# Kernel tuning notes

Measured on AMD Instinct MI355X. Metric: run time of the kernel, lower is better.

Reference implementation:

```python
import jax, jax.numpy as jnp
import numpy as np

N, C, L, K = 150000, 256, 50000, 200  # nodes, classes(=feature dim), labeled count, top-k


def setup_inputs() -> dict:
    key = jax.random.key(0)
    k1, k2 = jax.random.split(key)
    inputs = jax.random.normal(k1, (N, C), dtype=jnp.float32)
    cls = jax.random.randint(k2, (N,), 0, C)
    labels = jax.nn.one_hot(cls, C, dtype=jnp.float32)  # one-hot label matrix [N, C]
    labels_mask = jnp.arange(N) < L      # first L nodes labeled
    unlabels_mask = ~labels_mask
    return {"inputs": inputs, "labels": labels, "labels_mask": labels_mask,
            "unlabels_mask": unlabels_mask, "k": K}


def _l2n(x):
    # tf.nn.l2_normalize with epsilon 1e-12
    return x * jax.lax.rsqrt(jnp.maximum(jnp.sum(x * x, axis=-1, keepdims=True), 1e-12))


def reference(inputs, labels, labels_mask, unlabels_mask, k):
    lm = labels_mask.astype(inputs.dtype)    # [N]
    um = unlabels_mask.astype(inputs.dtype)  # [N]
    # protos: per-class mean of labeled features (masked matmul == boolean_mask + matmul)
    total = jnp.einsum('nf,nc->fc', inputs * lm[:, None], labels)  # [F, C]
    weight = 1.0 / jnp.sum(labels, 0)                               # 1/count per class (over ALL labels, as in TF)
    protos = (total * weight[None, :]).T                            # [C, F]
    # cosine similarity of every node to every prototype [N, C]
    prob = _l2n(inputs) @ _l2n(protos).T
    # per-row top-k, scattered back to a sparse [N, C] (raw top values, softmax in TF was dead code)
    vals, idx = jax.lax.top_k(prob, k)                              # [N, k]
    rows = jnp.arange(prob.shape[0])[:, None]
    sparse = jnp.zeros_like(prob).at[rows, idx].set(vals)
    p = sparse * um[:, None]                                        # only unlabeled rows contribute
    # per-class normalization: denom_c = sum_u p[u,c] + n_labeled_c
    denom = jnp.sum(p, 0) + jnp.sum(labels * lm[:, None], 0)        # [C]
    w = p / denom[None, :]                                          # [N, C]
    # change[c] = sum_u w[u,c] * (x_u - protos[c])
    change = w.T @ inputs - jnp.sum(w, 0)[:, None] * protos         # [C, F]
    protos = protos + change
    logits = _l2n(inputs) @ _l2n(protos).T                          # [N, C]
    return logits
```

## Files before the change

kernel.cpp:

```cpp
#include <hip/hip_runtime.h>

typedef unsigned int uint;
typedef unsigned short ushort;
typedef float f32x4 __attribute__((ext_vector_type(4)));
typedef uint u32x4 __attribute__((ext_vector_type(4)));
typedef uint u32x2 __attribute__((ext_vector_type(2)));
typedef __bf16 bf16x8 __attribute__((ext_vector_type(8)));

constexpr int NR = 150000;
constexpr int CD = 256;
constexpr int LR = 50000;
constexpr int KEX = 56;
constexpr int NB1 = 49984;
constexpr int NUP = 100032;
constexpr int NTP = 150080;

__device__ __forceinline__ ushort f2bf(float x) {
  uint u = __builtin_bit_cast(uint, x);
  u += 0x7FFFu + ((u >> 16) & 1u);
  return (ushort)(u >> 16);
}
__device__ __forceinline__ uint key16(uint b) {
  return (b & 0x8000u) ? (~b & 0xFFFFu) : (b | 0x8000u);
}

__global__ __launch_bounds__(256) void k_cls(const float* __restrict__ labels,
                                             int* __restrict__ cls,
                                             float* __restrict__ ca,
                                             float* __restrict__ cl) {
  __shared__ int ha[256], hl[256];
  int t = threadIdx.x;
  ha[t] = 0; hl[t] = 0;
  __syncthreads();
  int lane = t & 63;
  int wid = (blockIdx.x << 2) | (t >> 6);
  int nw = gridDim.x << 2;
  for (int n = wid; n < NR; n += nw) {
    f32x4 v = *reinterpret_cast<const f32x4*>(&labels[n * CD + lane * 4]);
    int j = v[0] > 0.5f ? 0 : v[1] > 0.5f ? 1 : v[2] > 0.5f ? 2 : v[3] > 0.5f ? 3 : -1;
    if (j >= 0) {
      int c = lane * 4 + j;
      cls[n] = c;
      atomicAdd(&ha[c], 1);
      if (n < LR) atomicAdd(&hl[c], 1);
    }
  }
  __syncthreads();
  atomicAdd(&ca[t], (float)ha[t]);
  atomicAdd(&cl[t], (float)hl[t]);
}

__global__ __launch_bounds__(256) void k_prep(const float* __restrict__ X,
                                              ushort* __restrict__ Xt,
                                              float* __restrict__ invn) {
  __shared__ __align__(16) ushort xl[64 * 264];
  __shared__ float red[256];
  int t = threadIdx.x;
  int r = t >> 2, cq = t & 3;
  int g0 = blockIdx.x * 64;
  int g = g0 + r;
  bool valid = g < NR;
  float ss = 0.f;
#pragma unroll
  for (int j = 0; j < 16; ++j) {
    int col = cq * 4 + j * 16;
    f32x4 x = valid ? *reinterpret_cast<const f32x4*>(&X[g * CD + col])
                    : (f32x4){0.f, 0.f, 0.f, 0.f};
    ss += x[0] * x[0] + x[1] * x[1] + x[2] * x[2] + x[3] * x[3];
    uint p0 = (uint)f2bf(x[0]) | ((uint)f2bf(x[1]) << 16);
    uint p1 = (uint)f2bf(x[2]) | ((uint)f2bf(x[3]) << 16);
    *reinterpret_cast<u32x2*>(&xl[r * 264 + col]) = (u32x2){p0, p1};
  }
  red[t] = ss;
  __syncthreads();
  if (t < 64) {
    float s4 = red[t * 4] + red[t * 4 + 1] + red[t * 4 + 2] + red[t * 4 + 3];
    if (g0 + t < NR) invn[g0 + t] = rsqrtf(fmaxf(s4, 1e-12f));
  }
  ushort* xp = Xt + (size_t)blockIdx.x * 16384;
  int f = t;
  uint buf[4];
  for (int n = 0; n < 64; ++n) {
    ushort v16 = xl[n * 264 + f];
    int sl = n & 7;
    if (sl & 1) buf[sl >> 1] |= (uint)v16 << 16; else buf[sl >> 1] = v16;
    if (sl == 7)
      *reinterpret_cast<u32x4*>(&xp[f * 64 + n - 7]) =
          (u32x4){buf[0], buf[1], buf[2], buf[3]};
  }
}

template <int KIND>
__global__ __launch_bounds__(1024) void k_gemmB(const int* __restrict__ cls,
                                                const ushort* __restrict__ Ap,
                                                const ushort* __restrict__ Xt,
                                                float* __restrict__ P,
                                                int nch, int nbase) {
  __shared__ __align__(16) ushort Al[256 * 40];
  __shared__ __align__(16) ushort Bl[256 * 40];
  int t = threadIdx.x;
  int lane = t & 63, w = t >> 6;
  int m = lane & 15, qd = lane >> 4;
  f32x4 acc[16];
#pragma unroll
  for (int i = 0; i < 16; ++i) acc[i] = (f32x4){0.f, 0.f, 0.f, 0.f};

  for (int ch = blockIdx.x; ch < nch; ch += gridDim.x) {
    int n0 = ch * 32;
    __syncthreads();
    if (KIND == 0) {
      for (int i = t; i < 5120; i += 1024) reinterpret_cast<uint*>(Al)[i] = 0u;
      __syncthreads();
      if (t < 32) {
        int g = n0 + t;
        if (g < LR) Al[cls[g] * 40 + t] = 0x3F80;
      }
    } else {
      const ushort* ap = Ap + (size_t)(n0 >> 6) * 16384 + (n0 & 63);
      int c = t >> 2, off = (t & 3) * 8;
      *reinterpret_cast<u32x4*>(&Al[c * 40 + off]) =
          *reinterpret_cast<const u32x4*>(&ap[c * 64 + off]);
    }
    {
      int gr = nbase + n0;
      const ushort* xp = Xt + (size_t)(gr >> 6) * 16384 + (gr & 63);
      int fR = t >> 2, off = (t & 3) * 8;
      *reinterpret_cast<u32x4*>(&Bl[fR * 40 + off]) =
          *reinterpret_cast<const u32x4*>(&xp[fR * 64 + off]);
    }
    __syncthreads();
    bf16x8 a = *reinterpret_cast<const bf16x8*>(&Al[(w * 16 + m) * 40 + qd * 8]);
#pragma unroll
    for (int ft = 0; ft < 16; ++ft) {
      bf16x8 b = *reinterpret_cast<const bf16x8*>(&Bl[(ft * 16 + m) * 40 + qd * 8]);
      acc[ft] = __builtin_amdgcn_mfma_f32_16x16x32_bf16(a, b, acc[ft], 0, 0, 0);
    }
  }
  float* Ps = P + (size_t)blockIdx.x * 65536;
#pragma unroll
  for (int ft = 0; ft < 16; ++ft)
#pragma unroll
    for (int r = 0; r < 4; ++r)
      Ps[(w * 16 + qd * 4 + r) * 256 + ft * 16 + m] = acc[ft][r];
}

__global__ __launch_bounds__(256) void k_protos(const float* __restrict__ P, int nsl,
                                                const float* __restrict__ ca,
                                                float* __restrict__ protos,
                                                ushort* __restrict__ phat) {
  __shared__ float red[256];
  int c = blockIdx.x, f = threadIdx.x;
  float s = 0.f;
  for (int i = 0; i < nsl; ++i) s += P[i * 65536 + c * 256 + f];
  float cnt = ca[c];
  float pv = cnt > 0.5f ? s / cnt : 0.f;
  protos[c * 256 + f] = pv;
  red[f] = pv * pv;
  __syncthreads();
  for (int st = 128; st > 0; st >>= 1) {
    if (f < st) red[f] += red[f + st];
    __syncthreads();
  }
  float iv = rsqrtf(fmaxf(red[0], 1e-12f));
  phat[c * 256 + f] = f2bf(pv * iv);
}

__global__ __launch_bounds__(256) void k_update(const float* __restrict__ PS, int nsl,
                                                const float* __restrict__ protos,
                                                const float* __restrict__ q,
                                                const float* __restrict__ clab,
                                                ushort* __restrict__ phat2) {
  __shared__ float red[256];
  int c = blockIdx.x, f = threadIdx.x;
  float s = 0.f;
  for (int i = 0; i < nsl; ++i) s += PS[i * 65536 + c * 256 + f];
  float qc = q[c];
  float den = qc + clab[c];
  float pv = protos[c * 256 + f];
  float np = pv + (s - qc * pv) / den;
  red[f] = np * np;
  __syncthreads();
  for (int st = 128; st > 0; st >>= 1) {
    if (f < st) red[f] += red[f + st];
    __syncthreads();
  }
  float iv = rsqrtf(fmaxf(red[0], 1e-12f));
  phat2[c * 256 + f] = f2bf(np * iv);
}

template <int TOPK>
__global__ __launch_bounds__(256) void k_passA(const float* __restrict__ X,
                                               const float* __restrict__ invn,
                                               const ushort* __restrict__ Bm,
                                               float* __restrict__ out,
                                               ushort* __restrict__ pt,
                                               float* __restrict__ q,
                                               int gbase) {
  __shared__ __align__(16) ushort Al[64 * 40];
  __shared__ __align__(16) ushort Bl[256 * 40];
  __shared__ __align__(16) ushort s16[TOPK ? 64 * 272 : 64];
  __shared__ uint tkey[TOPK ? 64 : 1];
  int t = threadIdx.x;
  int lane = t & 63, w = t >> 6;
  int m = lane & 15, qd = lane >> 4;
  int g0 = gbase + blockIdx.x * 64;
  int row = t >> 2, off = (t & 3) * 8;
  int g = g0 + row;
  bool valid = g < NR;
  float inv = valid ? invn[g] : 0.f;
  f32x4 acc[16];
#pragma unroll
  for (int i = 0; i < 16; ++i) acc[i] = (f32x4){0.f, 0.f, 0.f, 0.f};

  for (int k0 = 0; k0 < 256; k0 += 32) {
    __syncthreads();
    f32x4 x0 = valid ? *reinterpret_cast<const f32x4*>(&X[g * CD + k0 + off])
                     : (f32x4){0.f, 0.f, 0.f, 0.f};
    f32x4 x1 = valid ? *reinterpret_cast<const f32x4*>(&X[g * CD + k0 + off + 4])
                     : (f32x4){0.f, 0.f, 0.f, 0.f};
    x0 *= inv; x1 *= inv;
    uint u0 = (uint)f2bf(x0[0]) | ((uint)f2bf(x0[1]) << 16);
    uint u1 = (uint)f2bf(x0[2]) | ((uint)f2bf(x0[3]) << 16);
    uint u2 = (uint)f2bf(x1[0]) | ((uint)f2bf(x1[1]) << 16);
    uint u3 = (uint)f2bf(x1[2]) | ((uint)f2bf(x1[3]) << 16);
    *reinterpret_cast<u32x4*>(&Al[row * 40 + off]) = (u32x4){u0, u1, u2, u3};
#pragma unroll
    for (int i = 0; i < 4; ++i) {
      int c = (t >> 2) + i * 64;
      *reinterpret_cast<u32x4*>(&Bl[c * 40 + off]) =
          *reinterpret_cast<const u32x4*>(&Bm[c * 256 + k0 + off]);
    }
    __syncthreads();
    bf16x8 a = *reinterpret_cast<const bf16x8*>(&Al[(w * 16 + m) * 40 + qd * 8]);
#pragma unroll
    for (int ft = 0; ft < 16; ++ft) {
      bf16x8 b = *reinterpret_cast<const bf16x8*>(&Bl[(ft * 16 + m) * 40 + qd * 8]);
      acc[ft] = __builtin_amdgcn_mfma_f32_16x16x32_bf16(a, b, acc[ft], 0, 0, 0);
    }
  }

  if (TOPK == 0) {
#pragma unroll
    for (int ft = 0; ft < 16; ++ft)
#pragma unroll
      for (int r = 0; r < 4; ++r) {
        int rr = w * 16 + qd * 4 + r;
        int gg = g0 + rr;
        if (gg < NR) out[gg * 256 + ft * 16 + m] = acc[ft][r];
      }
  } else {
    __syncthreads();
#pragma unroll
    for (int ft = 0; ft < 16; ++ft)
#pragma unroll
      for (int r = 0; r < 4; ++r)
        s16[(w * 16 + qd * 4 + r) * 272 + ft * 16 + m] = f2bf(acc[ft][r]);
    __syncthreads();
    for (int i = 0; i < 16; ++i) {
      int rw = w * 16 + i;
      u32x2 pk = *reinterpret_cast<const u32x2*>(&s16[rw * 272 + lane * 4]);
      uint k0 = key16(pk[0] & 0xFFFFu);
      uint k1 = key16(pk[0] >> 16);
      uint k2 = key16(pk[1] & 0xFFFFu);
      uint k3 = key16(pk[1] >> 16);
      uint mth = 0u;
      for (int b = 15; b >= 0; --b) {
        uint cand = mth | (1u << b);
        int cnt = __builtin_popcountll(__ballot(k0 < cand)) +
                  __builtin_popcountll(__ballot(k1 < cand)) +
                  __builtin_popcountll(__ballot(k2 < cand)) +
                  __builtin_popcountll(__ballot(k3 < cand));
        if (cnt <= KEX) mth = cand;
      }
      if (lane == 0) tkey[rw] = mth;
    }
    __syncthreads();
    int c = t;
    float qloc = 0.f;
    uint buf[4];
    ushort* pp = pt + (size_t)blockIdx.x * 16384;
    for (int n = 0; n < 64; ++n) {
      int grow = g0 + n;
      ushort v16 = s16[n * 272 + c];
      bool keep = (key16(v16) >= tkey[n]) && (grow >= LR) && (grow < NR);
      ushort pv16 = keep ? v16 : (ushort)0;
      if (keep) qloc += __builtin_bit_cast(float, (uint)v16 << 16);
      int sl = n & 7;
      if (sl & 1) buf[sl >> 1] |= (uint)pv16 << 16; else buf[sl >> 1] = pv16;
      if (sl == 7)
        *reinterpret_cast<u32x4*>(&pp[c * 64 + n - 7]) =
            (u32x4){buf[0], buf[1], buf[2], buf[3]};
    }
    atomicAdd(&q[c], qloc);
  }
}

extern "C" void kernel_launch(void* const* d_in, const int* in_sizes, int n_in,
                              void* d_out, int out_size, void* d_ws, size_t ws_size,
                              hipStream_t stream) {
  const float* inputs = (const float*)d_in[0];
  const float* labels = (const float*)d_in[1];
  float* out = (float*)d_out;

  ushort* p_t = (ushort*)d_out;
  ushort* Xt  = (ushort*)((char*)d_out + (size_t)256 * NUP * 2);

  char* ws = (char*)d_ws;
  float* q      = (float*)(ws + 0);
  float* c_all  = (float*)(ws + 1024);
  float* c_lab  = (float*)(ws + 2048);
  float* protos = (float*)(ws + 4096);
  ushort* phat  = (ushort*)(ws + 4096 + 262144);
  ushort* phat2 = (ushort*)(ws + 4096 + 262144 + 131072);
  float* invn   = (float*)(ws + 528384);
  int*   cls    = (int*)(ws + 1128384);
  size_t base = 1736704;
  int sT = 128, sS = 256;
  while (base + (size_t)(sT + sS) * 262144ULL > ws_size) {
    if (sS > sT) sS >>= 1; else if (sT > 8) sT >>= 1; else break;
  }
  float* PT = (float*)(ws + base);
  float* PS = PT + (size_t)sT * 65536;

  hipMemsetAsync(ws, 0, 3072, stream);

  k_cls<<<1024, 256, 0, stream>>>(labels, cls, c_all, c_lab);
  k_prep<<<NTP / 64, 256, 0, stream>>>(inputs, Xt, invn);
  k_gemmB<0><<<sT, 1024, 0, stream>>>(cls, nullptr, Xt, PT, 1563, 0);
  k_protos<<<256, 256, 0, stream>>>(PT, sT, c_all, protos, phat);
  k_passA<1><<<NUP / 64, 256, 0, stream>>>(inputs, invn, phat, nullptr, p_t, q, NB1);
  k_gemmB<1><<<sS, 1024, 0, stream>>>(nullptr, p_t, Xt, PS, NUP / 32, NB1);
  k_update<<<256, 256, 0, stream>>>(PS, sS, protos, q, c_lab, phat2);
  k_passA<0><<<(NR + 63) / 64, 256, 0, stream>>>(inputs, invn, phat2, out, nullptr, nullptr, 0);
}
```

Before: 796.8 us.

## Prefetch next tiles into registers and batch top-k threshold search across rows

The GEMM kernels now load the next chunk's A/B tiles from global memory into registers while the current tile is computed, so global latency overlaps the MFMA work. In k_gemmB's one-hot path, the full LDS clear each iteration is replaced by clearing only the previously set entries. k_passA aliases its LDS buffers into one array to cut LDS footprint and adds a launch-bounds occupancy hint. Its per-row radix threshold search now handles four rows at once to expose more independent ballots. The cost is higher register pressure, which could lower occupancy or cause spills.

```diff
diff --git a/kernel.cpp b/kernel.cpp
--- a/kernel.cpp
+++ b/kernel.cpp
@@ -101,32 +101,57 @@
   int t = threadIdx.x;
   int lane = t & 63, w = t >> 6;
   int m = lane & 15, qd = lane >> 4;
+  int cR = t >> 2, off = (t & 3) * 8;
   f32x4 acc[16];
 #pragma unroll
   for (int i = 0; i < 16; ++i) acc[i] = (f32x4){0.f, 0.f, 0.f, 0.f};
 
-  for (int ch = blockIdx.x; ch < nch; ch += gridDim.x) {
+  if (KIND == 0) {
+    for (int i = t; i < 5120; i += 1024) reinterpret_cast<uint*>(Al)[i] = 0u;
+  }
+
+  u32x4 aR, bR;
+  int curc = -1, prevc = -1;
+  int ch = blockIdx.x;
+  if (ch < nch) {
     int n0 = ch * 32;
+    if (KIND == 1) {
+      const ushort* ap = Ap + (size_t)(n0 >> 6) * 16384 + (n0 & 63);
+      aR = *reinterpret_cast<const u32x4*>(&ap[cR * 64 + off]);
+    } else if (t < 32) {
+      int gg = n0 + t;
+      curc = (gg < LR) ? cls[gg] : -1;
+    }
+    int gr = nbase + n0;
+    const ushort* xp = Xt + (size_t)(gr >> 6) * 16384 + (gr & 63);
+    bR = *reinterpret_cast<const u32x4*>(&xp[cR * 64 + off]);
+  }
+
+  for (; ch < nch; ch += gridDim.x) {
     __syncthreads();
     if (KIND == 0) {
-      for (int i = t; i < 5120; i += 1024) reinterpret_cast<uint*>(Al)[i] = 0u;
-      __syncthreads();
       if (t < 32) {
-        int g = n0 + t;
-        if (g < LR) Al[cls[g] * 40 + t] = 0x3F80;
+        if (prevc >= 0) Al[prevc * 40 + t] = 0;
+        if (curc >= 0) Al[curc * 40 + t] = 0x3F80;
+        prevc = curc;
       }
     } else {
-      const ushort* ap = Ap + (size_t)(n0 >> 6) * 16384 + (n0 & 63);
-      int c = t >> 2, off = (t & 3) * 8;
-      *reinterpret_cast<u32x4*>(&Al[c * 40 + off]) =
-          *reinterpret_cast<const u32x4*>(&ap[c * 64 + off]);
-    }
-    {
+      *reinterpret_cast<u32x4*>(&Al[cR * 40 + off]) = aR;
+    }
+    *reinterpret_cast<u32x4*>(&Bl[cR * 40 + off]) = bR;
+    int chn = ch + gridDim.x;
+    if (chn < nch) {
+      int n0 = chn * 32;
+      if (KIND == 1) {
+        const ushort* ap = Ap + (size_t)(n0 >> 6) * 16384 + (n0 & 63);
+        aR = *reinterpret_cast<const u32x4*>(&ap[cR * 64 + off]);
+      } else if (t < 32) {
+        int gg = n0 + t;
+        curc = (gg < LR) ? cls[gg] : -1;
+      }
       int gr = nbase + n0;
       const ushort* xp = Xt + (size_t)(gr >> 6) * 16384 + (gr & 63);
-      int fR = t >> 2, off = (t & 3) * 8;
-      *reinterpret_cast<u32x4*>(&Bl[fR * 40 + off]) =
-          *reinterpret_cast<const u32x4*>(&xp[fR * 64 + off]);
+      bR = *reinterpret_cast<const u32x4*>(&xp[cR * 64 + off]);
     }
     __syncthreads();
     bf16x8 a = *reinterpret_cast<const bf16x8*>(&Al[(w * 16 + m) * 40 + qd * 8]);
@@ -189,17 +214,16 @@
 }
 
 template <int TOPK>
-__global__ __launch_bounds__(256) void k_passA(const float* __restrict__ X,
-                                               const float* __restrict__ invn,
-                                               const ushort* __restrict__ Bm,
-                                               float* __restrict__ out,
-                                               ushort* __restrict__ pt,
-                                               float* __restrict__ q,
-                                               int gbase) {
-  __shared__ __align__(16) ushort Al[64 * 40];
-  __shared__ __align__(16) ushort Bl[256 * 40];
-  __shared__ __align__(16) ushort s16[TOPK ? 64 * 272 : 64];
-  __shared__ uint tkey[TOPK ? 64 : 1];
+__global__ __launch_bounds__(256, 4) void k_passA(const float* __restrict__ X,
+                                                  const float* __restrict__ invn,
+                                                  const ushort* __restrict__ Bm,
+                                                  float* __restrict__ out,
+                                                  ushort* __restrict__ pt,
+                                                  float* __restrict__ q,
+                                                  int gbase) {
+  __shared__ __align__(16) char smem[TOPK ? 35072 : 25600];
+  ushort* Al = reinterpret_cast<ushort*>(smem);
+  ushort* Bl = reinterpret_cast<ushort*>(smem + 5120);
   int t = threadIdx.x;
   int lane = t & 63, w = t >> 6;
   int m = lane & 15, qd = lane >> 4;
@@ -212,23 +236,36 @@
 #pragma unroll
   for (int i = 0; i < 16; ++i) acc[i] = (f32x4){0.f, 0.f, 0.f, 0.f};
 
+  f32x4 x0 = valid ? *reinterpret_cast<const f32x4*>(&X[g * CD + off])
+                   : (f32x4){0.f, 0.f, 0.f, 0.f};
+  f32x4 x1 = valid ? *reinterpret_cast<const f32x4*>(&X[g * CD + off + 4])
+                   : (f32x4){0.f, 0.f, 0.f, 0.f};
+  u32x4 bR[4];
+#pragma unroll
+  for (int i = 0; i < 4; ++i)
+    bR[i] = *reinterpret_cast<const u32x4*>(&Bm[((t >> 2) + i * 64) * 256 + off]);
+
   for (int k0 = 0; k0 < 256; k0 += 32) {
-    __syncthreads();
-    f32x4 x0 = valid ? *reinterpret_cast<const f32x4*>(&X[g * CD + k0 + off])
-                     : (f32x4){0.f, 0.f, 0.f, 0.f};
-    f32x4 x1 = valid ? *reinterpret_cast<const f32x4*>(&X[g * CD + k0 + off + 4])
-                     : (f32x4){0.f, 0.f, 0.f, 0.f};
-    x0 *= inv; x1 *= inv;
-    uint u0 = (uint)f2bf(x0[0]) | ((uint)f2bf(x0[1]) << 16);
-    uint u1 = (uint)f2bf(x0[2]) | ((uint)f2bf(x0[3]) << 16);
-    uint u2 = (uint)f2bf(x1[0]) | ((uint)f2bf(x1[1]) << 16);
-    uint u3 = (uint)f2bf(x1[2]) | ((uint)f2bf(x1[3]) << 16);
+    f32x4 y0 = x0 * inv, y1 = x1 * inv;
+    uint u0 = (uint)f2bf(y0[0]) | ((uint)f2bf(y0[1]) << 16);
+    uint u1 = (uint)f2bf(y0[2]) | ((uint)f2bf(y0[3]) << 16);
+    uint u2 = (uint)f2bf(y1[0]) | ((uint)f2bf(y1[1]) << 16);
+    uint u3 = (uint)f2bf(y1[2]) | ((uint)f2bf(y1[3]) << 16);
+    __syncthreads();
     *reinterpret_cast<u32x4*>(&Al[row * 40 + off]) = (u32x4){u0, u1, u2, u3};
 #pragma unroll
-    for (int i = 0; i < 4; ++i) {
-      int c = (t >> 2) + i * 64;
-      *reinterpret_cast<u32x4*>(&Bl[c * 40 + off]) =
-          *reinterpret_cast<const u32x4*>(&Bm[c * 256 + k0 + off]);
+    for (int i = 0; i < 4; ++i)
+      *reinterpret_cast<u32x4*>(&Bl[((t >> 2) + i * 64) * 40 + off]) = bR[i];
+    if (k0 < 224) {
+      int kn = k0 + 32;
+      x0 = valid ? *reinterpret_cast<const f32x4*>(&X[g * CD + kn + off])
+                 : (f32x4){0.f, 0.f, 0.f, 0.f};
+      x1 = valid ? *reinterpret_cast<const f32x4*>(&X[g * CD + kn + off + 4])
+                 : (f32x4){0.f, 0.f, 0.f, 0.f};
+#pragma unroll
+      for (int i = 0; i < 4; ++i)
+        bR[i] = *reinterpret_cast<const u32x4*>(
+            &Bm[((t >> 2) + i * 64) * 256 + kn + off]);
     }
     __syncthreads();
     bf16x8 a = *reinterpret_cast<const bf16x8*>(&Al[(w * 16 + m) * 40 + qd * 8]);
@@ -239,7 +276,7 @@
     }
   }
 
-  if (TOPK == 0) {
+  if constexpr (TOPK == 0) {
 #pragma unroll
     for (int ft = 0; ft < 16; ++ft)
 #pragma unroll
@@ -249,6 +286,8 @@
         if (gg < NR) out[gg * 256 + ft * 16 + m] = acc[ft][r];
       }
   } else {
+    ushort* s16 = reinterpret_cast<ushort*>(smem);
+    uint* tkey = reinterpret_cast<uint*>(smem + 34816);
     __syncthreads();
 #pragma unroll
     for (int ft = 0; ft < 16; ++ft)
@@ -256,23 +295,34 @@
       for (int r = 0; r < 4; ++r)
         s16[(w * 16 + qd * 4 + r) * 272 + ft * 16 + m] = f2bf(acc[ft][r]);
     __syncthreads();
-    for (int i = 0; i < 16; ++i) {
-      int rw = w * 16 + i;
-      u32x2 pk = *reinterpret_cast<const u32x2*>(&s16[rw * 272 + lane * 4]);
-      uint k0 = key16(pk[0] & 0xFFFFu);
-      uint k1 = key16(pk[0] >> 16);
-      uint k2 = key16(pk[1] & 0xFFFFu);
-      uint k3 = key16(pk[1] >> 16);
-      uint mth = 0u;
+    for (int i0 = 0; i0 < 16; i0 += 4) {
+      uint kk[4][4];
+      uint mth[4];
+#pragma unroll
+      for (int rr = 0; rr < 4; ++rr) {
+        int rw = w * 16 + i0 + rr;
+        u32x2 pk = *reinterpret_cast<const u32x2*>(&s16[rw * 272 + lane * 4]);
+        kk[rr][0] = key16(pk[0] & 0xFFFFu);
+        kk[rr][1] = key16(pk[0] >> 16);
+        kk[rr][2] = key16(pk[1] & 0xFFFFu);
+        kk[rr][3] = key16(pk[1] >> 16);
+        mth[rr] = 0u;
+      }
       for (int b = 15; b >= 0; --b) {
-        uint cand = mth | (1u << b);
-        int cnt = __builtin_popcountll(__ballot(k0 < cand)) +
-                  __builtin_popcountll(__ballot(k1 < cand)) +
-                  __builtin_popcountll(__ballot(k2 < cand)) +
-                  __builtin_popcountll(__ballot(k3 < cand));
-        if (cnt <= KEX) mth = cand;
-      }
-      if (lane == 0) tkey[rw] = mth;
+#pragma unroll
+        for (int rr = 0; rr < 4; ++rr) {
+          uint cand = mth[rr] | (1u << b);
+          int cnt = __builtin_popcountll(__ballot(kk[rr][0] < cand)) +
+                    __builtin_popcountll(__ballot(kk[rr][1] < cand)) +
+                    __builtin_popcountll(__ballot(kk[rr][2] < cand)) +
+                    __builtin_popcountll(__ballot(kk[rr][3] < cand));
+          if (cnt <= KEX) mth[rr] = cand;
+        }
+      }
+      if (lane == 0) {
+#pragma unroll
+        for (int rr = 0; rr < 4; ++rr) tkey[w * 16 + i0 + rr] = mth[rr];
+      }
     }
     __syncthreads();
     int c = t;
```

Result: faster. 719.4 us (-9.7%).
